# Performance work log

Hardware: AMD Instinct MI355X
Metric: run time of the kernel (lower is better)

## Reference

```python
import jax, jax.numpy as jnp
import numpy as np

THRESHOLD = 0.4
TOPK = 4


def _box_iou(boxes1, boxes2):
    # boxes1: [B, Q, 4], boxes2: [B, G, 4] in (x1, y1, x2, y2)
    area1 = (boxes1[..., 2] - boxes1[..., 0]) * (boxes1[..., 3] - boxes1[..., 1])  # [B,Q]
    area2 = (boxes2[..., 2] - boxes2[..., 0]) * (boxes2[..., 3] - boxes2[..., 1])  # [B,G]
    lt = jnp.maximum(boxes1[:, :, None, :2], boxes2[:, None, :, :2])  # [B,Q,G,2]
    rb = jnp.minimum(boxes1[:, :, None, 2:], boxes2[:, None, :, 2:])  # [B,Q,G,2]
    wh = jnp.clip(rb - lt, 0.0)
    inter = wh[..., 0] * wh[..., 1]                                   # [B,Q,G]
    union = area1[:, :, None] + area2[:, None, :] - inter
    return inter / (union + 1e-07)


def _make_boxes(key, b, n):
    k1, k2 = jax.random.split(key)
    xy = jax.random.uniform(k1, (b, n, 2), dtype=jnp.float32) * 0.8
    wh = jax.random.uniform(k2, (b, n, 2), dtype=jnp.float32) * 0.2 + 0.01
    return jnp.concatenate([xy, xy + wh], axis=-1)  # valid x1<x2, y1<y2


def setup_inputs() -> dict:
    key = jax.random.key(0)
    k1, k2, k3 = jax.random.split(key, 3)
    B, Q, G = 128, 1000, 300
    pred_logits = jax.random.normal(k1, (B, Q, 1), dtype=jnp.float32)
    pred_boxes_xyxy = _make_boxes(k2, B, Q)
    tgt_boxes_xyxy = _make_boxes(k3, B, G)
    return {
        "pred_logits": pred_logits,
        "pred_boxes_xyxy": pred_boxes_xyxy,
        "tgt_boxes_xyxy": tgt_boxes_xyxy,
    }


def reference(pred_logits, pred_boxes_xyxy, tgt_boxes_xyxy):
    # Per-query binary score.
    score = jax.nn.sigmoid(pred_logits)[..., 0]              # [B,Q]
    iou = _box_iou(pred_boxes_xyxy, tgt_boxes_xyxy)          # [B,Q,G]
    valid = (iou > THRESHOLD).astype(score.dtype)
    gt_score = score[:, :, None] * iou * valid               # [B,Q,G]
    # Per-GT top-k over queries (same matches as the nested-loop original:
    # invalid entries are zero, and positives-only are kept via the mask).
    vals, idxs = jax.lax.top_k(jnp.swapaxes(gt_score, 1, 2), TOPK)  # [B,G,K]
    mask = vals > 0.0                                        # valid match mask
    return vals, idxs.astype(jnp.int32), mask
```

## Files before the change

kernel.cpp:

```cpp
#include <hip/hip_runtime.h>

#define NB 128
#define NQ 1000
#define NG 300
#define NK 4
#define THRESH 0.4f

#define GCHUNKS  12
#define GPERB    25
#define NTHREADS 256
#define CAP      48

__global__ __launch_bounds__(NTHREADS) void fused_matcher(
    const float* __restrict__ logits,
    const float* __restrict__ pboxes,
    const float* __restrict__ tboxes,
    float* __restrict__ out_vals,
    float* __restrict__ out_idx,
    float* __restrict__ out_mask)
{
    __shared__ float4 stb[GPERB + 1];
    __shared__ unsigned scnt[GPERB];
    __shared__ unsigned short sslot[GPERB][CAP];

    const int b   = blockIdx.y;
    const int gc  = blockIdx.x;
    const int tid = threadIdx.x;
    const int g0  = gc * GPERB;

    const float4* __restrict__ tb4 =
        reinterpret_cast<const float4*>(tboxes) + (size_t)b * NG + g0;
    const float4* __restrict__ pb4 =
        reinterpret_cast<const float4*>(pboxes) + (size_t)b * NQ;

    if (tid < GPERB) {
        stb[tid]  = tb4[tid];
        scnt[tid] = 0u;
    }
    if (tid == GPERB) stb[GPERB] = make_float4(2e9f, 2e9f, 2e9f, 2e9f);

    const float4 dummy = make_float4(2e9f, 2e9f, 2e9f, 2e9f);
    float4 pA = pb4[tid];
    float4 pB = pb4[NTHREADS + tid];
    float4 pC = pb4[2 * NTHREADS + tid];
    float4 pD = (3 * NTHREADS + tid < NQ) ? pb4[3 * NTHREADS + tid] : dummy;
    const float aA = 0.999f * ((pA.z - pA.x) * (pA.w - pA.y));
    const float aB = 0.999f * ((pB.z - pB.x) * (pB.w - pB.y));
    const float aC = 0.999f * ((pC.z - pC.x) * (pC.w - pC.y));
    const float aD = 0.999f * ((pD.z - pD.x) * (pD.w - pD.y));

    __syncthreads();

    unsigned mA = 0u, mB = 0u, mC = 0u, mD = 0u;
    float4 tc = stb[0];
#define TEST(P, A, M)                                                       \
    {                                                                       \
        float ltx = fmaxf(P.x, tc.x);                                       \
        float lty = fmaxf(P.y, tc.y);                                       \
        float rbx = fminf(P.z, tc.z);                                       \
        float rby = fminf(P.w, tc.w);                                       \
        float w = fmaxf(rbx - ltx, 0.0f);                                   \
        float h = fmaxf(rby - lty, 0.0f);                                   \
        float inter = w * h;                                                \
        unsigned pass = (fmaf(inter, 3.5f, -(A)) >= ta999) ? 1u : 0u;       \
        M = (M << 1) | pass;                                                \
    }
#pragma unroll
    for (int gi = 0; gi < GPERB; ++gi) {
        float4 tn = stb[gi + 1];
        const float ta999 = 0.999f * ((tc.z - tc.x) * (tc.w - tc.y));
        TEST(pA, aA, mA)
        TEST(pB, aB, mB)
        TEST(pC, aC, mC)
        TEST(pD, aD, mD)
        tc = tn;
    }
#undef TEST

#define DRAIN(M, SLOT)                                                      \
    while (M) {                                                             \
        int p  = __ffs(M) - 1;                                              \
        M &= M - 1u;                                                        \
        int gi = (GPERB - 1) - p;                                           \
        unsigned pos = atomicAdd(&scnt[gi], 1u);                            \
        if (pos < CAP)                                                      \
            sslot[gi][pos] = (unsigned short)((SLOT)*NTHREADS + tid);       \
    }
    DRAIN(mA, 0) DRAIN(mB, 1) DRAIN(mC, 2) DRAIN(mD, 3)
#undef DRAIN
    __syncthreads();

    const int grp = tid >> 2;
    const int l4  = tid & 3;
    if (grp < GPERB) {
        const float4 tb = stb[grp];
        const float tarea = (tb.z - tb.x) * (tb.w - tb.y);
        int n = (int)scnt[grp];
        if (n > CAP) n = CAP;
        const float* __restrict__ lg = logits + (size_t)b * NQ;

        unsigned long long k0 = 0ull, k1 = 0ull, k2 = 0ull, k3 = 0ull;
        for (int i = l4; i < n; i += 4) {
            const int q = sslot[grp][i];
            const float4 pp = pb4[q];
            float parea = (pp.z - pp.x) * (pp.w - pp.y);
            float ltx = fmaxf(pp.x, tb.x);
            float lty = fmaxf(pp.y, tb.y);
            float rbx = fminf(pp.z, tb.z);
            float rby = fminf(pp.w, tb.w);
            float w = fmaxf(rbx - ltx, 0.0f);
            float h = fmaxf(rby - lty, 0.0f);
            float inter = w * h;
            float uni   = parea + tarea - inter;
            float iou   = inter / (uni + 1e-7f);
            if (iou > THRESH) {
                float x   = lg[q];
                float sc  = 1.0f / (1.0f + expf(-x));
                float val = sc * iou;
                unsigned long long ck =
                    ((unsigned long long)__float_as_uint(val) << 32) |
                    (unsigned long long)(unsigned)(~(unsigned)q);
                if (ck > k3) {
                    if (ck > k0)      { k3 = k2; k2 = k1; k1 = k0; k0 = ck; }
                    else if (ck > k1) { k3 = k2; k2 = k1; k1 = ck; }
                    else if (ck > k2) { k3 = k2; k2 = ck; }
                    else              { k3 = ck; }
                }
            }
        }

#define MERGE_STEP(MASK)                                                    \
        {                                                                   \
            unsigned long long p0 = __shfl_xor(k0, MASK, 64);               \
            unsigned long long p1 = __shfl_xor(k1, MASK, 64);               \
            unsigned long long p2 = __shfl_xor(k2, MASK, 64);               \
            unsigned long long p3 = __shfl_xor(k3, MASK, 64);               \
            k0 = k0 > p3 ? k0 : p3;                                         \
            k1 = k1 > p2 ? k1 : p2;                                         \
            k2 = k2 > p1 ? k2 : p1;                                         \
            k3 = k3 > p0 ? k3 : p0;                                         \
            unsigned long long t;                                           \
            if (k0 < k2) { t = k0; k0 = k2; k2 = t; }                       \
            if (k1 < k3) { t = k1; k1 = k3; k3 = t; }                       \
            if (k0 < k1) { t = k0; k0 = k1; k1 = t; }                       \
            if (k2 < k3) { t = k2; k2 = k3; k3 = t; }                       \
        }
        MERGE_STEP(1)
        MERGE_STEP(2)
#undef MERGE_STEP

        if (l4 == 0) {
            const int iq0 = k0 ? (int)~(unsigned)k0 : -1;
            const int iq1 = k1 ? (int)~(unsigned)k1 : -1;
            const int iq2 = k2 ? (int)~(unsigned)k2 : -1;
            float4 vv, vi, vm;
            float* pv = &vv.x; float* pi_ = &vi.x; float* pm = &vm.x;
            int fill = 0;
#define EMIT(J, KJ)                                                         \
            {                                                               \
                if (KJ != 0ull) {                                           \
                    pv[J]  = __uint_as_float((unsigned)(KJ >> 32));         \
                    pi_[J] = (float)(int)~(unsigned)KJ;                     \
                    pm[J]  = 1.0f;                                          \
                } else {                                                    \
                    while (fill == iq0 || fill == iq1 || fill == iq2)       \
                        ++fill;                                             \
                    pv[J]  = 0.0f;                                          \
                    pi_[J] = (float)fill;                                   \
                    pm[J]  = 0.0f;                                          \
                    ++fill;                                                 \
                }                                                           \
            }
            EMIT(0, k0) EMIT(1, k1) EMIT(2, k2) EMIT(3, k3)
#undef EMIT
            const size_t o4 = (size_t)b * NG + g0 + grp;
            reinterpret_cast<float4*>(out_vals)[o4] = vv;
            reinterpret_cast<float4*>(out_idx)[o4]  = vi;
            reinterpret_cast<float4*>(out_mask)[o4] = vm;
        }
    }
}

extern "C" void kernel_launch(void* const* d_in, const int* in_sizes, int n_in,
                              void* d_out, int out_size, void* d_ws, size_t ws_size,
                              hipStream_t stream) {
    const float* logits = (const float*)d_in[0];
    const float* pboxes = (const float*)d_in[1];
    const float* tboxes = (const float*)d_in[2];

    float* out = (float*)d_out;
    const size_t bgk = (size_t)NB * NG * NK;
    float* out_vals = out;
    float* out_idx  = out + bgk;
    float* out_mask = out + 2 * bgk;

    dim3 grid(GCHUNKS, NB);
    fused_matcher<<<grid, NTHREADS, 0, stream>>>(logits, pboxes, tboxes,
                                                 out_vals, out_idx, out_mask);
}
```

Before: 35.01 us.

## Use 512-thread blocks with 38 GTs each and inline atomic candidate append

Reorganizes the grid to 8 GT chunks of 38 per batch with 512 threads, so each thread tests two queries instead of four. The bitmask-and-drain pass is replaced by an atomic append to the per-GT shared-memory list right inside the test loop. The top-k phase uses 8 lanes per GT with an extra shuffle merge step. Fewer blocks means less redundant loading of the prediction boxes, but it adds divergent atomics inside the loop and padding work for the partial last chunk.

```diff
diff --git a/kernel.cpp b/kernel.cpp
--- a/kernel.cpp
+++ b/kernel.cpp
@@ -6,12 +6,12 @@
 #define NK 4
 #define THRESH 0.4f
 
-#define GCHUNKS  12
-#define GPERB    25
-#define NTHREADS 256
+#define GCHUNKS  8
+#define GPERB    38
+#define NTHREADS 512
 #define CAP      48
 
-__global__ __launch_bounds__(NTHREADS) void fused_matcher(
+__global__ __launch_bounds__(NTHREADS, 8) void fused_matcher(
     const float* __restrict__ logits,
     const float* __restrict__ pboxes,
     const float* __restrict__ tboxes,
@@ -27,72 +27,59 @@
     const int gc  = blockIdx.x;
     const int tid = threadIdx.x;
     const int g0  = gc * GPERB;
+    const int ng  = (NG - g0 < GPERB) ? (NG - g0) : GPERB;
 
     const float4* __restrict__ tb4 =
         reinterpret_cast<const float4*>(tboxes) + (size_t)b * NG + g0;
     const float4* __restrict__ pb4 =
         reinterpret_cast<const float4*>(pboxes) + (size_t)b * NQ;
 
+    const float4 dummyG = make_float4(2e9f, 2e9f, 2e9f, 2e9f);
+    const float4 dummyQ = make_float4(2e9f, 2e9f, -2e9f, -2e9f);
+
     if (tid < GPERB) {
-        stb[tid]  = tb4[tid];
+        stb[tid]  = (tid < ng) ? tb4[tid] : dummyG;
         scnt[tid] = 0u;
     }
-    if (tid == GPERB) stb[GPERB] = make_float4(2e9f, 2e9f, 2e9f, 2e9f);
+    if (tid == GPERB) stb[GPERB] = dummyG;
 
-    const float4 dummy = make_float4(2e9f, 2e9f, 2e9f, 2e9f);
     float4 pA = pb4[tid];
-    float4 pB = pb4[NTHREADS + tid];
-    float4 pC = pb4[2 * NTHREADS + tid];
-    float4 pD = (3 * NTHREADS + tid < NQ) ? pb4[3 * NTHREADS + tid] : dummy;
-    const float aA = 0.999f * ((pA.z - pA.x) * (pA.w - pA.y));
-    const float aB = 0.999f * ((pB.z - pB.x) * (pB.w - pB.y));
-    const float aC = 0.999f * ((pC.z - pC.x) * (pC.w - pC.y));
-    const float aD = 0.999f * ((pD.z - pD.x) * (pD.w - pD.y));
+    float4 pB = (NTHREADS + tid < NQ) ? pb4[NTHREADS + tid] : dummyQ;
+    const float qaA = 0.999f * ((pA.z - pA.x) * (pA.w - pA.y));
+    const float qaB = 0.999f * ((pB.z - pB.x) * (pB.w - pB.y));
 
     __syncthreads();
 
-    unsigned mA = 0u, mB = 0u, mC = 0u, mD = 0u;
     float4 tc = stb[0];
-#define TEST(P, A, M)                                                       \
-    {                                                                       \
-        float ltx = fmaxf(P.x, tc.x);                                       \
-        float lty = fmaxf(P.y, tc.y);                                       \
-        float rbx = fminf(P.z, tc.z);                                       \
-        float rby = fminf(P.w, tc.w);                                       \
-        float w = fmaxf(rbx - ltx, 0.0f);                                   \
-        float h = fmaxf(rby - lty, 0.0f);                                   \
-        float inter = w * h;                                                \
-        unsigned pass = (fmaf(inter, 3.5f, -(A)) >= ta999) ? 1u : 0u;       \
-        M = (M << 1) | pass;                                                \
-    }
-#pragma unroll
     for (int gi = 0; gi < GPERB; ++gi) {
         float4 tn = stb[gi + 1];
         const float ta999 = 0.999f * ((tc.z - tc.x) * (tc.w - tc.y));
-        TEST(pA, aA, mA)
-        TEST(pB, aB, mB)
-        TEST(pC, aC, mC)
-        TEST(pD, aD, mD)
+
+#define TEST(P, QA, QIDX)                                                   \
+        {                                                                   \
+            float ltx = fmaxf(P.x, tc.x);                                   \
+            float lty = fmaxf(P.y, tc.y);                                   \
+            float rbx = fminf(P.z, tc.z);                                   \
+            float rby = fminf(P.w, tc.w);                                   \
+            float w = fmaxf(rbx - ltx, 0.0f);                               \
+            float h = fmaxf(rby - lty, 0.0f);                               \
+            float inter = w * h;                                            \
+            if (fmaf(inter, 3.5f, -(QA)) >= ta999) {                        \
+                unsigned pos = atomicAdd(&scnt[gi], 1u);                    \
+                if (pos < CAP)                                              \
+                    sslot[gi][pos] = (unsigned short)(QIDX);                \
+            }                                                               \
+        }
+        TEST(pA, qaA, tid)
+        TEST(pB, qaB, NTHREADS + tid)
+#undef TEST
         tc = tn;
     }
-#undef TEST
-
-#define DRAIN(M, SLOT)                                                      \
-    while (M) {                                                             \
-        int p  = __ffs(M) - 1;                                              \
-        M &= M - 1u;                                                        \
-        int gi = (GPERB - 1) - p;                                           \
-        unsigned pos = atomicAdd(&scnt[gi], 1u);                            \
-        if (pos < CAP)                                                      \
-            sslot[gi][pos] = (unsigned short)((SLOT)*NTHREADS + tid);       \
-    }
-    DRAIN(mA, 0) DRAIN(mB, 1) DRAIN(mC, 2) DRAIN(mD, 3)
-#undef DRAIN
     __syncthreads();
 
-    const int grp = tid >> 2;
-    const int l4  = tid & 3;
-    if (grp < GPERB) {
+    const int grp = tid >> 3;
+    const int l8  = tid & 7;
+    if (grp < ng) {
         const float4 tb = stb[grp];
         const float tarea = (tb.z - tb.x) * (tb.w - tb.y);
         int n = (int)scnt[grp];
@@ -100,7 +87,7 @@
         const float* __restrict__ lg = logits + (size_t)b * NQ;
 
         unsigned long long k0 = 0ull, k1 = 0ull, k2 = 0ull, k3 = 0ull;
-        for (int i = l4; i < n; i += 4) {
+        for (int i = l8; i < n; i += 8) {
             const int q = sslot[grp][i];
             const float4 pp = pb4[q];
             float parea = (pp.z - pp.x) * (pp.w - pp.y);
@@ -147,9 +134,10 @@
         }
         MERGE_STEP(1)
         MERGE_STEP(2)
+        MERGE_STEP(4)
 #undef MERGE_STEP
 
-        if (l4 == 0) {
+        if (l8 == 0) {
             const int iq0 = k0 ? (int)~(unsigned)k0 : -1;
             const int iq1 = k1 ? (int)~(unsigned)k1 : -1;
             const int iq2 = k2 ? (int)~(unsigned)k2 : -1;
```

Result: slower. 49.59 us (+41.6%).
